# Optimization experiments

Hardware: AMD Instinct MI355X
Metric: run time of the kernel (lower is better)

## Reference

```python
import jax, jax.numpy as jnp
import numpy as np

N = 50000
E = 800000
IN_C = 32
HID = 64
OUT_C = 1
EPS = 1e-5


def setup_inputs() -> dict:
    key = jax.random.key(0)
    ks = jax.random.split(key, 16)
    x = jax.random.normal(ks[0], (N, IN_C), dtype=jnp.float32)
    edge_index = jax.random.randint(ks[1], (2, E), 0, N, dtype=jnp.int64)
    s = 0.1
    return {
        "x": x,
        "edge_index": edge_index,
        # SAGEConv1: lin_l (on aggregated neighbors, with bias), lin_r (on root, no bias)
        "W1l": jax.random.normal(ks[2], (IN_C, HID), dtype=jnp.float32) * s,
        "b1l": jnp.zeros((HID,), dtype=jnp.float32),
        "W1r": jax.random.normal(ks[3], (IN_C, HID), dtype=jnp.float32) * s,
        "bn1_g": jnp.ones((HID,), dtype=jnp.float32),
        "bn1_b": jnp.zeros((HID,), dtype=jnp.float32),
        "bn1_m": jax.random.normal(ks[4], (HID,), dtype=jnp.float32) * s,
        "bn1_v": jax.random.uniform(ks[5], (HID,), dtype=jnp.float32, minval=0.5, maxval=1.5),
        "W2l": jax.random.normal(ks[6], (HID, HID), dtype=jnp.float32) * s,
        "b2l": jnp.zeros((HID,), dtype=jnp.float32),
        "W2r": jax.random.normal(ks[7], (HID, HID), dtype=jnp.float32) * s,
        "bn2_g": jnp.ones((HID,), dtype=jnp.float32),
        "bn2_b": jnp.zeros((HID,), dtype=jnp.float32),
        "bn2_m": jax.random.normal(ks[8], (HID,), dtype=jnp.float32) * s,
        "bn2_v": jax.random.uniform(ks[9], (HID,), dtype=jnp.float32, minval=0.5, maxval=1.5),
        "Wlin": jax.random.normal(ks[10], (HID, OUT_C), dtype=jnp.float32) * s,
        "blin": jnp.zeros((OUT_C,), dtype=jnp.float32),
    }


def _sage_conv(x, src, dst, Wl, bl, Wr, deg_inv):
    # mean aggregation of source features onto destination nodes
    agg = jax.ops.segment_sum(x[src], dst, num_segments=N)  # [N, C]
    agg = agg * deg_inv[:, None]
    return agg @ Wl + bl + x @ Wr


def _bn_eval(x, g, b, m, v):
    return (x - m) * (g * jax.lax.rsqrt(v + EPS)) + b


def reference(x, edge_index, W1l, b1l, W1r, bn1_g, bn1_b, bn1_m, bn1_v,
              W2l, b2l, W2r, bn2_g, bn2_b, bn2_m, bn2_v, Wlin, blin):
    src, dst = edge_index[0], edge_index[1]
    deg = jax.ops.segment_sum(jnp.ones((E,), jnp.float32), dst, num_segments=N)
    deg_inv = 1.0 / jnp.maximum(deg, 1.0)

    h = _sage_conv(x, src, dst, W1l, b1l, W1r, deg_inv)
    h = jax.nn.relu(_bn_eval(h, bn1_g, bn1_b, bn1_m, bn1_v))
    # dropout p=0.5 in eval mode -> identity
    h = _sage_conv(h, src, dst, W2l, b2l, W2r, deg_inv)
    h = jax.nn.relu(_bn_eval(h, bn2_g, bn2_b, bn2_m, bn2_v))
    return h @ Wlin + blin
```

## Files before the change

kernel.cpp:

```cpp
#include <hip/hip_runtime.h>


constexpr int NN = 50000;
constexpr int NE = 800000;
constexpr int NBLK = (NN + 63) / 64;
constexpr float BN_EPS = 1e-5f;

constexpr int NBUCK = 196;
constexpr int BCAP  = 8192;
constexpr int APB   = 2048;
constexpr int NAB   = (NE + APB - 1) / APB;

__global__ __launch_bounds__(256) void k_binA(const int* __restrict__ ei,
                                              int* __restrict__ cursor,
                                              unsigned int* __restrict__ region) {
    __shared__ int lcnt[NBUCK];
    __shared__ int gb[NBUCK];
    int tid = threadIdx.x;
    for (int i = tid; i < NBUCK; i += 256) lcnt[i] = 0;
    __syncthreads();
    int e0 = blockIdx.x * APB;
    unsigned int pk[8];
    int bk[8], rk[8];
#pragma unroll
    for (int i = 0; i < 8; i++) {
        int e = e0 + i * 256 + tid;
        bk[i] = -1;
        if (e < NE) {
            int s = ei[e];
            int d = ei[NE + e];
            pk[i] = ((unsigned int)d << 16) | (unsigned int)s;
            bk[i] = d >> 8;
            rk[i] = atomicAdd(&lcnt[bk[i]], 1);
        }
    }
    __syncthreads();
    if (tid < NBUCK && lcnt[tid] > 0) gb[tid] = atomicAdd(&cursor[tid], lcnt[tid]);
    __syncthreads();
#pragma unroll
    for (int i = 0; i < 8; i++) {
        if (bk[i] >= 0) region[bk[i] * BCAP + gb[bk[i]] + rk[i]] = pk[i];
    }
}

__global__ __launch_bounds__(256) void k_binB(const int* __restrict__ cursor,
                                              const unsigned int* __restrict__ region,
                                              int* __restrict__ deg_i,
                                              int* __restrict__ base,
                                              unsigned short* __restrict__ csr16) {
    __shared__ unsigned int stg[BCAP];
    __shared__ int lc[256], cur[256], sctmp[256];
    int tid = threadIdx.x;
    int b = blockIdx.x;

    int cntt = (tid < NBUCK) ? cursor[tid] : 0;
    sctmp[tid] = cntt;
    __syncthreads();
    for (int off = 1; off < 256; off <<= 1) {
        int t = (tid >= off) ? sctmp[tid - off] : 0;
        __syncthreads();
        sctmp[tid] += t;
        __syncthreads();
    }
    int B0 = (b == 0) ? 0 : sctmp[b - 1];
    int mycnt = cursor[b];

    for (int k = tid; k < mycnt; k += 256) stg[k] = region[b * BCAP + k];
    lc[tid] = 0;
    __syncthreads();

    int node0 = b << 8;
    for (int k = tid; k < mycnt; k += 256) {
        int local = (int)(stg[k] >> 16) - node0;
        atomicAdd(&lc[local], 1);
    }
    __syncthreads();

    int myc = lc[tid];
    sctmp[tid] = myc;
    __syncthreads();
    for (int off = 1; off < 256; off <<= 1) {
        int t = (tid >= off) ? sctmp[tid - off] : 0;
        __syncthreads();
        sctmp[tid] += t;
        __syncthreads();
    }
    int myoff = sctmp[tid] - myc;
    cur[tid] = myoff;
    int n = node0 + tid;
    if (n < NN) {
        deg_i[n] = myc;
        base[n] = B0 + myoff + myc;
    }
    __syncthreads();

    for (int k = tid; k < mycnt; k += 256) {
        unsigned int p = stg[k];
        int local = (int)(p >> 16) - node0;
        int pos = atomicAdd(&cur[local], 1);
        csr16[B0 + pos] = (unsigned short)(p & 0xffffu);
    }
}

__global__ __launch_bounds__(256) void k_gather32(const unsigned short* __restrict__ csr_src,
                                                  const int* __restrict__ base,
                                                  const int* __restrict__ deg_i,
                                                  const float* __restrict__ x,
                                                  float* __restrict__ agg) {
    int t = blockIdx.x * 256 + threadIdx.x;
    int n = t >> 5;
    if (n >= NN) return;
    int p = (t >> 3) & 3;
    int c4 = (t & 7) << 2;
    int end = base[n];
    int st = end - deg_i[n];
    float4 acc = make_float4(0.f, 0.f, 0.f, 0.f);
    for (int e = st + p; e < end; e += 4) {
        int s = csr_src[e];
        float4 v = *(const float4*)(x + (size_t)s * 32 + c4);
        acc.x += v.x; acc.y += v.y; acc.z += v.z; acc.w += v.w;
    }
    acc.x += __shfl_xor(acc.x, 8, 64);
    acc.y += __shfl_xor(acc.y, 8, 64);
    acc.z += __shfl_xor(acc.z, 8, 64);
    acc.w += __shfl_xor(acc.w, 8, 64);
    acc.x += __shfl_xor(acc.x, 16, 64);
    acc.y += __shfl_xor(acc.y, 16, 64);
    acc.z += __shfl_xor(acc.z, 16, 64);
    acc.w += __shfl_xor(acc.w, 16, 64);
    if (p == 0) *(float4*)(agg + (size_t)n * 32 + c4) = acc;
}

__global__ __launch_bounds__(256) void k_gather64(const unsigned short* __restrict__ csr_src,
                                                  const int* __restrict__ base,
                                                  const int* __restrict__ deg_i,
                                                  const float* __restrict__ h,
                                                  float* __restrict__ agg) {
    int t = blockIdx.x * 256 + threadIdx.x;
    int n = t >> 6;
    if (n >= NN) return;
    int p = (t >> 4) & 3;
    int c4 = (t & 15) << 2;
    int end = base[n];
    int st = end - deg_i[n];
    float4 acc = make_float4(0.f, 0.f, 0.f, 0.f);
    for (int e = st + p; e < end; e += 4) {
        int s = csr_src[e];
        float4 v = *(const float4*)(h + (size_t)s * 64 + c4);
        acc.x += v.x; acc.y += v.y; acc.z += v.z; acc.w += v.w;
    }
    acc.x += __shfl_xor(acc.x, 16, 64);
    acc.y += __shfl_xor(acc.y, 16, 64);
    acc.z += __shfl_xor(acc.z, 16, 64);
    acc.w += __shfl_xor(acc.w, 16, 64);
    acc.x += __shfl_xor(acc.x, 32, 64);
    acc.y += __shfl_xor(acc.y, 32, 64);
    acc.z += __shfl_xor(acc.z, 32, 64);
    acc.w += __shfl_xor(acc.w, 32, 64);
    if (p == 0) *(float4*)(agg + (size_t)n * 64 + c4) = acc;
}

__global__ __launch_bounds__(256) void k_node1(
    const float* __restrict__ x, const float* __restrict__ agg,
    const int* __restrict__ deg_i,
    const float* __restrict__ W1l, const float* __restrict__ b1l,
    const float* __restrict__ W1r,
    const float* __restrict__ g1, const float* __restrict__ bb1,
    const float* __restrict__ m1, const float* __restrict__ v1,
    float* __restrict__ h) {
    __shared__ float wlds[32 * 128];
    int tid = threadIdx.x;
    {
        const float4* l4 = (const float4*)W1l;
        const float4* r4 = (const float4*)W1r;
        float4* s4 = (float4*)wlds;
#pragma unroll
        for (int i = 0; i < 2; i++) {
            int idx = tid + i * 256;
            int k = idx >> 4, c = idx & 15;
            s4[k * 32 + c] = l4[idx];
            s4[k * 32 + 16 + c] = r4[idx];
        }
    }
    __syncthreads();

    int lg = tid & 15, o4 = lg << 2;
    int nbase = blockIdx.x * 64 + (tid >> 4) * 4;
    if (nbase >= NN) return;

    float4 acc[4];
    float di[4];
    int nj[4];
#pragma unroll
    for (int j = 0; j < 4; j++) {
        acc[j] = make_float4(0.f, 0.f, 0.f, 0.f);
        nj[j] = min(nbase + j, NN - 1);
        di[j] = 1.0f / fmaxf((float)deg_i[nj[j]], 1.0f);
    }

#pragma unroll 4
    for (int i4 = 0; i4 < 32; i4 += 4) {
        float4 wl[4], wr[4];
#pragma unroll
        for (int k = 0; k < 4; k++) {
            wl[k] = *(const float4*)&wlds[(i4 + k) * 128 + o4];
            wr[k] = *(const float4*)&wlds[(i4 + k) * 128 + 64 + o4];
        }
#pragma unroll
        for (int j = 0; j < 4; j++) {
            float4 a4 = *(const float4*)(agg + (size_t)nj[j] * 32 + i4);
            float4 x4 = *(const float4*)(x + (size_t)nj[j] * 32 + i4);
            float av[4] = {a4.x * di[j], a4.y * di[j], a4.z * di[j], a4.w * di[j]};
            float xv[4] = {x4.x, x4.y, x4.z, x4.w};
#pragma unroll
            for (int k = 0; k < 4; k++) {
                acc[j].x += av[k] * wl[k].x + xv[k] * wr[k].x;
                acc[j].y += av[k] * wl[k].y + xv[k] * wr[k].y;
                acc[j].z += av[k] * wl[k].z + xv[k] * wr[k].z;
                acc[j].w += av[k] * wl[k].w + xv[k] * wr[k].w;
            }
        }
    }

    float4 bl = *(const float4*)(b1l + o4);
    float4 gg = *(const float4*)(g1 + o4);
    float4 bb = *(const float4*)(bb1 + o4);
    float4 mm = *(const float4*)(m1 + o4);
    float4 vv = *(const float4*)(v1 + o4);
    float4 sc;
    sc.x = gg.x * rsqrtf(vv.x + BN_EPS);
    sc.y = gg.y * rsqrtf(vv.y + BN_EPS);
    sc.z = gg.z * rsqrtf(vv.z + BN_EPS);
    sc.w = gg.w * rsqrtf(vv.w + BN_EPS);
#pragma unroll
    for (int j = 0; j < 4; j++) {
        if (nbase + j >= NN) break;
        float4 r;
        r.x = fmaxf((acc[j].x + bl.x - mm.x) * sc.x + bb.x, 0.0f);
        r.y = fmaxf((acc[j].y + bl.y - mm.y) * sc.y + bb.y, 0.0f);
        r.z = fmaxf((acc[j].z + bl.z - mm.z) * sc.z + bb.z, 0.0f);
        r.w = fmaxf((acc[j].w + bl.w - mm.w) * sc.w + bb.w, 0.0f);
        *(float4*)(h + (size_t)(nbase + j) * 64 + o4) = r;
    }
}

__global__ __launch_bounds__(256) void k_node2(
    const float* __restrict__ h, const float* __restrict__ agg,
    const int* __restrict__ deg_i,
    const float* __restrict__ W2l, const float* __restrict__ b2l,
    const float* __restrict__ W2r,
    const float* __restrict__ g2, const float* __restrict__ bb2,
    const float* __restrict__ m2, const float* __restrict__ v2,
    const float* __restrict__ Wlin, const float* __restrict__ blin,
    float* __restrict__ out) {
    __shared__ float wlds[64 * 128];
    int tid = threadIdx.x;
    {
        const float4* l4 = (const float4*)W2l;
        const float4* r4 = (const float4*)W2r;
        float4* s4 = (float4*)wlds;
#pragma unroll
        for (int i = 0; i < 4; i++) {
            int idx = tid + i * 256;
            int k = idx >> 4, c = idx & 15;
            s4[k * 32 + c] = l4[idx];
            s4[k * 32 + 16 + c] = r4[idx];
        }
    }
    __syncthreads();

    int lg = tid & 15, o4 = lg << 2;
    int nbase = blockIdx.x * 64 + (tid >> 4) * 4;
    if (nbase >= NN) return;

    float4 acc[4];
    float di[4];
    int nj[4];
#pragma unroll
    for (int j = 0; j < 4; j++) {
        acc[j] = make_float4(0.f, 0.f, 0.f, 0.f);
        nj[j] = min(nbase + j, NN - 1);
        di[j] = 1.0f / fmaxf((float)deg_i[nj[j]], 1.0f);
    }

#pragma unroll 4
    for (int i4 = 0; i4 < 64; i4 += 4) {
        float4 wl[4], wr[4];
#pragma unroll
        for (int k = 0; k < 4; k++) {
            wl[k] = *(const float4*)&wlds[(i4 + k) * 128 + o4];
            wr[k] = *(const float4*)&wlds[(i4 + k) * 128 + 64 + o4];
        }
#pragma unroll
        for (int j = 0; j < 4; j++) {
            float4 a4 = *(const float4*)(agg + (size_t)nj[j] * 64 + i4);
            float4 h4 = *(const float4*)(h + (size_t)nj[j] * 64 + i4);
            float av[4] = {a4.x * di[j], a4.y * di[j], a4.z * di[j], a4.w * di[j]};
            float hv[4] = {h4.x, h4.y, h4.z, h4.w};
#pragma unroll
            for (int k = 0; k < 4; k++) {
                acc[j].x += av[k] * wl[k].x + hv[k] * wr[k].x;
                acc[j].y += av[k] * wl[k].y + hv[k] * wr[k].y;
                acc[j].z += av[k] * wl[k].z + hv[k] * wr[k].z;
                acc[j].w += av[k] * wl[k].w + hv[k] * wr[k].w;
            }
        }
    }

    float4 bl = *(const float4*)(b2l + o4);
    float4 gg = *(const float4*)(g2 + o4);
    float4 bb = *(const float4*)(bb2 + o4);
    float4 mm = *(const float4*)(m2 + o4);
    float4 vv = *(const float4*)(v2 + o4);
    float4 wo = *(const float4*)(Wlin + o4);
    float blin0 = blin[0];
    float4 sc;
    sc.x = gg.x * rsqrtf(vv.x + BN_EPS);
    sc.y = gg.y * rsqrtf(vv.y + BN_EPS);
    sc.z = gg.z * rsqrtf(vv.z + BN_EPS);
    sc.w = gg.w * rsqrtf(vv.w + BN_EPS);
#pragma unroll
    for (int j = 0; j < 4; j++) {
        float vx = fmaxf((acc[j].x + bl.x - mm.x) * sc.x + bb.x, 0.0f);
        float vy = fmaxf((acc[j].y + bl.y - mm.y) * sc.y + bb.y, 0.0f);
        float vz = fmaxf((acc[j].z + bl.z - mm.z) * sc.z + bb.z, 0.0f);
        float vw = fmaxf((acc[j].w + bl.w - mm.w) * sc.w + bb.w, 0.0f);
        float part = vx * wo.x + vy * wo.y + vz * wo.z + vw * wo.w;
#pragma unroll
        for (int m = 1; m < 16; m <<= 1) part += __shfl_xor(part, m, 64);
        if (lg == 0 && nbase + j < NN) out[nbase + j] = part + blin0;
    }
}

extern "C" void kernel_launch(void* const* d_in, const int* in_sizes, int n_in,
                              void* d_out, int out_size, void* d_ws, size_t ws_size,
                              hipStream_t stream) {
    const float* x    = (const float*)d_in[0];
    const int*   ei   = (const int*)d_in[1];
    const float* W1l  = (const float*)d_in[2];
    const float* b1l  = (const float*)d_in[3];
    const float* W1r  = (const float*)d_in[4];
    const float* g1   = (const float*)d_in[5];
    const float* bb1  = (const float*)d_in[6];
    const float* m1   = (const float*)d_in[7];
    const float* v1   = (const float*)d_in[8];
    const float* W2l  = (const float*)d_in[9];
    const float* b2l  = (const float*)d_in[10];
    const float* W2r  = (const float*)d_in[11];
    const float* g2   = (const float*)d_in[12];
    const float* bb2  = (const float*)d_in[13];
    const float* m2   = (const float*)d_in[14];
    const float* v2   = (const float*)d_in[15];
    const float* Wlin = (const float*)d_in[16];
    const float* blin = (const float*)d_in[17];
    float* out = (float*)d_out;

    int* cursor = (int*)d_ws;
    unsigned int* region = (unsigned int*)(cursor + 256);
    int* deg_i = (int*)(region + (size_t)NBUCK * BCAP);
    int* base  = deg_i + NN;
    unsigned short* csr16 = (unsigned short*)(base + NN);
    float* agg = (float*)(csr16 + NE);
    float* h   = agg + (size_t)64 * NN;

    hipMemsetAsync(cursor, 0, 256 * sizeof(int), stream);

    k_binA<<<NAB, 256, 0, stream>>>(ei, cursor, region);
    k_binB<<<NBUCK, 256, 0, stream>>>(cursor, region, deg_i, base, csr16);

    k_gather32<<<(NN * 32 + 255) / 256, 256, 0, stream>>>(csr16, base, deg_i, x, agg);
    k_node1<<<NBLK, 256, 0, stream>>>(x, agg, deg_i, W1l, b1l, W1r,
                                      g1, bb1, m1, v1, h);
    k_gather64<<<(NN * 64 + 255) / 256, 256, 0, stream>>>(csr16, base, deg_i, h, agg);
    k_node2<<<NBLK, 256, 0, stream>>>(h, agg, deg_i, W2l, b2l, W2r,
                                      g2, bb2, m2, v2, Wlin, blin, out);
}
```

Measured before the change: 214.0 us.

## Fuse neighbor gathers into node kernels and store hidden features as bf16

```diff
diff --git a/kernel.cpp b/kernel.cpp
--- a/kernel.cpp
+++ b/kernel.cpp
@@ -10,6 +10,13 @@
 constexpr int BCAP  = 8192;
 constexpr int APB   = 2048;
 constexpr int NAB   = (NE + APB - 1) / APB;
+
+__device__ __forceinline__ unsigned short f2bf(float f) {
+    union { float f; unsigned int u; } c; c.f = f;
+    unsigned int lsb = (c.u >> 16) & 1u;
+    c.u += 0x7fffu + lsb;
+    return (unsigned short)(c.u >> 16);
+}
 
 __global__ __launch_bounds__(256) void k_binA(const int* __restrict__ ei,
                                               int* __restrict__ cursor,
@@ -102,73 +109,17 @@
     }
 }
 
-__global__ __launch_bounds__(256) void k_gather32(const unsigned short* __restrict__ csr_src,
-                                                  const int* __restrict__ base,
-                                                  const int* __restrict__ deg_i,
-                                                  const float* __restrict__ x,
-                                                  float* __restrict__ agg) {
-    int t = blockIdx.x * 256 + threadIdx.x;
-    int n = t >> 5;
-    if (n >= NN) return;
-    int p = (t >> 3) & 3;
-    int c4 = (t & 7) << 2;
-    int end = base[n];
-    int st = end - deg_i[n];
-    float4 acc = make_float4(0.f, 0.f, 0.f, 0.f);
-    for (int e = st + p; e < end; e += 4) {
-        int s = csr_src[e];
-        float4 v = *(const float4*)(x + (size_t)s * 32 + c4);
-        acc.x += v.x; acc.y += v.y; acc.z += v.z; acc.w += v.w;
-    }
-    acc.x += __shfl_xor(acc.x, 8, 64);
-    acc.y += __shfl_xor(acc.y, 8, 64);
-    acc.z += __shfl_xor(acc.z, 8, 64);
-    acc.w += __shfl_xor(acc.w, 8, 64);
-    acc.x += __shfl_xor(acc.x, 16, 64);
-    acc.y += __shfl_xor(acc.y, 16, 64);
-    acc.z += __shfl_xor(acc.z, 16, 64);
-    acc.w += __shfl_xor(acc.w, 16, 64);
-    if (p == 0) *(float4*)(agg + (size_t)n * 32 + c4) = acc;
-}
-
-__global__ __launch_bounds__(256) void k_gather64(const unsigned short* __restrict__ csr_src,
-                                                  const int* __restrict__ base,
-                                                  const int* __restrict__ deg_i,
-                                                  const float* __restrict__ h,
-                                                  float* __restrict__ agg) {
-    int t = blockIdx.x * 256 + threadIdx.x;
-    int n = t >> 6;
-    if (n >= NN) return;
-    int p = (t >> 4) & 3;
-    int c4 = (t & 15) << 2;
-    int end = base[n];
-    int st = end - deg_i[n];
-    float4 acc = make_float4(0.f, 0.f, 0.f, 0.f);
-    for (int e = st + p; e < end; e += 4) {
-        int s = csr_src[e];
-        float4 v = *(const float4*)(h + (size_t)s * 64 + c4);
-        acc.x += v.x; acc.y += v.y; acc.z += v.z; acc.w += v.w;
-    }
-    acc.x += __shfl_xor(acc.x, 16, 64);
-    acc.y += __shfl_xor(acc.y, 16, 64);
-    acc.z += __shfl_xor(acc.z, 16, 64);
-    acc.w += __shfl_xor(acc.w, 16, 64);
-    acc.x += __shfl_xor(acc.x, 32, 64);
-    acc.y += __shfl_xor(acc.y, 32, 64);
-    acc.z += __shfl_xor(acc.z, 32, 64);
-    acc.w += __shfl_xor(acc.w, 32, 64);
-    if (p == 0) *(float4*)(agg + (size_t)n * 64 + c4) = acc;
-}
-
-__global__ __launch_bounds__(256) void k_node1(
-    const float* __restrict__ x, const float* __restrict__ agg,
-    const int* __restrict__ deg_i,
+__global__ __launch_bounds__(256) void k_fused1(
+    const float* __restrict__ x,
+    const unsigned short* __restrict__ csr16,
+    const int* __restrict__ base, const int* __restrict__ deg_i,
     const float* __restrict__ W1l, const float* __restrict__ b1l,
     const float* __restrict__ W1r,
     const float* __restrict__ g1, const float* __restrict__ bb1,
     const float* __restrict__ m1, const float* __restrict__ v1,
-    float* __restrict__ h) {
+    unsigned short* __restrict__ h) {
     __shared__ float wlds[32 * 128];
+    __shared__ float aggs[64 * 32];
     int tid = threadIdx.x;
     {
         const float4* l4 = (const float4*)W1l;
@@ -182,19 +133,36 @@
             s4[k * 32 + 16 + c] = r4[idx];
         }
     }
+    int nb0 = blockIdx.x * 64;
+#pragma unroll
+    for (int g = 0; g < 2; g++) {
+        int nl = g * 32 + (tid >> 3);
+        int c4 = (tid & 7) << 2;
+        int nc = min(nb0 + nl, NN - 1);
+        int end = base[nc];
+        int st = end - deg_i[nc];
+        float4 acc = make_float4(0.f, 0.f, 0.f, 0.f);
+        for (int e = st; e < end; e++) {
+            int s = csr16[e];
+            float4 v = *(const float4*)(x + (size_t)s * 32 + c4);
+            acc.x += v.x; acc.y += v.y; acc.z += v.z; acc.w += v.w;
+        }
+        *(float4*)&aggs[nl * 32 + c4] = acc;
+    }
     __syncthreads();
 
     int lg = tid & 15, o4 = lg << 2;
-    int nbase = blockIdx.x * 64 + (tid >> 4) * 4;
+    int nbase = nb0 + (tid >> 4) * 4;
     if (nbase >= NN) return;
 
     float4 acc[4];
     float di[4];
-    int nj[4];
+    int nj[4], njl[4];
 #pragma unroll
     for (int j = 0; j < 4; j++) {
         acc[j] = make_float4(0.f, 0.f, 0.f, 0.f);
         nj[j] = min(nbase + j, NN - 1);
+        njl[j] = nj[j] - nb0;
         di[j] = 1.0f / fmaxf((float)deg_i[nj[j]], 1.0f);
     }
 
@@ -208,7 +176,7 @@
         }
 #pragma unroll
         for (int j = 0; j < 4; j++) {
-            float4 a4 = *(const float4*)(agg + (size_t)nj[j] * 32 + i4);
+            float4 a4 = *(const float4*)&aggs[njl[j] * 32 + i4];
             float4 x4 = *(const float4*)(x + (size_t)nj[j] * 32 + i4);
             float av[4] = {a4.x * di[j], a4.y * di[j], a4.z * di[j], a4.w * di[j]};
             float xv[4] = {x4.x, x4.y, x4.z, x4.w};
@@ -235,18 +203,19 @@
 #pragma unroll
     for (int j = 0; j < 4; j++) {
         if (nbase + j >= NN) break;
-        float4 r;
-        r.x = fmaxf((acc[j].x + bl.x - mm.x) * sc.x + bb.x, 0.0f);
-        r.y = fmaxf((acc[j].y + bl.y - mm.y) * sc.y + bb.y, 0.0f);
-        r.z = fmaxf((acc[j].z + bl.z - mm.z) * sc.z + bb.z, 0.0f);
-        r.w = fmaxf((acc[j].w + bl.w - mm.w) * sc.w + bb.w, 0.0f);
-        *(float4*)(h + (size_t)(nbase + j) * 64 + o4) = r;
-    }
-}
-
-__global__ __launch_bounds__(256) void k_node2(
-    const float* __restrict__ h, const float* __restrict__ agg,
-    const int* __restrict__ deg_i,
+        ushort4 r;
+        r.x = f2bf(fmaxf((acc[j].x + bl.x - mm.x) * sc.x + bb.x, 0.0f));
+        r.y = f2bf(fmaxf((acc[j].y + bl.y - mm.y) * sc.y + bb.y, 0.0f));
+        r.z = f2bf(fmaxf((acc[j].z + bl.z - mm.z) * sc.z + bb.z, 0.0f));
+        r.w = f2bf(fmaxf((acc[j].w + bl.w - mm.w) * sc.w + bb.w, 0.0f));
+        *(ushort4*)(h + (size_t)(nbase + j) * 64 + o4) = r;
+    }
+}
+
+__global__ __launch_bounds__(256) void k_fused2(
+    const unsigned short* __restrict__ h,
+    const unsigned short* __restrict__ csr16,
+    const int* __restrict__ base, const int* __restrict__ deg_i,
     const float* __restrict__ W2l, const float* __restrict__ b2l,
     const float* __restrict__ W2r,
     const float* __restrict__ g2, const float* __restrict__ bb2,
@@ -254,6 +223,7 @@
     const float* __restrict__ Wlin, const float* __restrict__ blin,
     float* __restrict__ out) {
     __shared__ float wlds[64 * 128];
+    __shared__ float aggs[64 * 64];
     int tid = threadIdx.x;
     {
         const float4* l4 = (const float4*)W2l;
@@ -267,19 +237,45 @@
             s4[k * 32 + 16 + c] = r4[idx];
         }
     }
+    int nb0 = blockIdx.x * 64;
+#pragma unroll
+    for (int g = 0; g < 2; g++) {
+        int nl = g * 32 + (tid >> 3);
+        int c8 = (tid & 7) << 3;
+        int nc = min(nb0 + nl, NN - 1);
+        int end = base[nc];
+        int st = end - deg_i[nc];
+        float a0 = 0.f, a1 = 0.f, a2 = 0.f, a3 = 0.f;
+        float a4 = 0.f, a5 = 0.f, a6 = 0.f, a7 = 0.f;
+        for (int e = st; e < end; e++) {
+            int s = csr16[e];
+            uint4 v = *(const uint4*)(h + (size_t)s * 64 + c8);
+            a0 += __uint_as_float(v.x << 16);
+            a1 += __uint_as_float(v.x & 0xffff0000u);
+            a2 += __uint_as_float(v.y << 16);
+            a3 += __uint_as_float(v.y & 0xffff0000u);
+            a4 += __uint_as_float(v.z << 16);
+            a5 += __uint_as_float(v.z & 0xffff0000u);
+            a6 += __uint_as_float(v.w << 16);
+            a7 += __uint_as_float(v.w & 0xffff0000u);
+        }
+        *(float4*)&aggs[nl * 64 + c8]     = make_float4(a0, a1, a2, a3);
+        *(float4*)&aggs[nl * 64 + c8 + 4] = make_float4(a4, a5, a6, a7);
+    }
     __syncthreads();
 
     int lg = tid & 15, o4 = lg << 2;
-    int nbase = blockIdx.x * 64 + (tid >> 4) * 4;
+    int nbase = nb0 + (tid >> 4) * 4;
     if (nbase >= NN) return;
 
     float4 acc[4];
     float di[4];
-    int nj[4];
+    int nj[4], njl[4];
 #pragma unroll
     for (int j = 0; j < 4; j++) {
         acc[j] = make_float4(0.f, 0.f, 0.f, 0.f);
         nj[j] = min(nbase + j, NN - 1);
+        njl[j] = nj[j] - nb0;
         di[j] = 1.0f / fmaxf((float)deg_i[nj[j]], 1.0f);
     }
 
@@ -293,10 +289,14 @@
         }
 #pragma unroll
         for (int j = 0; j < 4; j++) {
-            float4 a4 = *(const float4*)(agg + (size_t)nj[j] * 64 + i4);
-            float4 h4 = *(const float4*)(h + (size_t)nj[j] * 64 + i4);
-            float av[4] = {a4.x * di[j], a4.y * di[j], a4.z * di[j], a4.w * di[j]};
-            float hv[4] = {h4.x, h4.y, h4.z, h4.w};
+            float4 ag = *(const float4*)&aggs[njl[j] * 64 + i4];
+            uint2 hu = *(const uint2*)(h + (size_t)nj[j] * 64 + i4);
+            float av[4] = {ag.x * di[j], ag.y * di[j], ag.z * di[j], ag.w * di[j]};
+            float hv[4];
+            hv[0] = __uint_as_float(hu.x << 16);
+            hv[1] = __uint_as_float(hu.x & 0xffff0000u);
+            hv[2] = __uint_as_float(hu.y << 16);
+            hv[3] = __uint_as_float(hu.y & 0xffff0000u);
 #pragma unroll
             for (int k = 0; k < 4; k++) {
                 acc[j].x += av[k] * wl[k].x + hv[k] * wr[k].x;
@@ -360,18 +360,14 @@
     int* deg_i = (int*)(region + (size_t)NBUCK * BCAP);
     int* base  = deg_i + NN;
     unsigned short* csr16 = (unsigned short*)(base + NN);
-    float* agg = (float*)(csr16 + NE);
-    float* h   = agg + (size_t)64 * NN;
+    unsigned short* h = csr16 + NE;
 
     hipMemsetAsync(cursor, 0, 256 * sizeof(int), stream);
 
     k_binA<<<NAB, 256, 0, stream>>>(ei, cursor, region);
     k_binB<<<NBUCK, 256, 0, stream>>>(cursor, region, deg_i, base, csr16);
-
-    k_gather32<<<(NN * 32 + 255) / 256, 256, 0, stream>>>(csr16, base, deg_i, x, agg);
-    k_node1<<<NBLK, 256, 0, stream>>>(x, agg, deg_i, W1l, b1l, W1r,
-                                      g1, bb1, m1, v1, h);
-    k_gather64<<<(NN * 64 + 255) / 256, 256, 0, stream>>>(csr16, base, deg_i, h, agg);
-    k_node2<<<NBLK, 256, 0, stream>>>(h, agg, deg_i, W2l, b2l, W2r,
-                                      g2, bb2, m2, v2, Wlin, blin, out);
-}
+    k_fused1<<<NBLK, 256, 0, stream>>>(x, csr16, base, deg_i, W1l, b1l, W1r,
+                                       g1, bb1, m1, v1, h);
+    k_fused2<<<NBLK, 256, 0, stream>>>(h, csr16, base, deg_i, W2l, b2l, W2r,
+                                       g2, bb2, m2, v2, Wlin, blin, out);
+}
```

Result: slower. 255.2 us (+19.3%).
